# Performance work log

Measured on AMD Instinct MI355X. Metric: run time of the kernel, lower is better.

The kernel has to match this reference:

```python
import jax, jax.numpy as jnp
import numpy as np

B, C, N, D, H, NC = 128, 9, 2048, 192, 384, 18  # batch, in_chans, time, embed, mlp_hidden, classes


def setup_inputs() -> dict:
    key = jax.random.key(0)
    ks = jax.random.split(key, 18)
    rn = lambda k, sh, s=0.02: jax.random.normal(k, sh, dtype=jnp.float32) * s
    return {
        "x": jax.random.normal(ks[0], (B, C, N), dtype=jnp.float32),
        "conv_w": rn(ks[1], (D, C, 3)),
        "conv_b": jnp.zeros((D,), jnp.float32),
        "pos_embed": jnp.zeros((1, N, D), jnp.float32),
        "qkv_w": rn(ks[2], (3 * D, D)),
        "qkv_b": jnp.zeros((3 * D,), jnp.float32),
        "proj_w": rn(ks[3], (D, D)),
        "proj_b": jnp.zeros((D,), jnp.float32),
        "ln1_g": jnp.ones((D,), jnp.float32),
        "ln1_b": jnp.zeros((D,), jnp.float32),
        "mlp_w1": rn(ks[4], (H, D)),
        "mlp_b1": jnp.zeros((H,), jnp.float32),
        "mlp_w2": rn(ks[5], (D, H)),
        "mlp_b2": jnp.zeros((D,), jnp.float32),
        "ln2_g": jnp.ones((D,), jnp.float32),
        "ln2_b": jnp.zeros((D,), jnp.float32),
        "head_w": rn(ks[6], (NC, D)),
        "head_b": jnp.zeros((NC,), jnp.float32),
    }


def _ln(x, g, b, eps=1e-5):
    m = x.mean(-1, keepdims=True)
    v = ((x - m) ** 2).mean(-1, keepdims=True)
    return (x - m) * jax.lax.rsqrt(v + eps) * g + b


def reference(x, conv_w, conv_b, pos_embed, qkv_w, qkv_b, proj_w, proj_b,
              ln1_g, ln1_b, mlp_w1, mlp_b1, mlp_w2, mlp_b2, ln2_g, ln2_b,
              head_w, head_b):
    # patch embed: Conv1d(C->D, k=3, pad=1), then [B, N, D]
    h = jax.lax.conv_general_dilated(
        x, conv_w, window_strides=(1,), padding=[(1, 1)],
        dimension_numbers=("NCH", "OIH", "NCH")) + conv_b[None, :, None]
    h = jnp.transpose(h, (0, 2, 1)) + pos_embed  # [B, N, D]

    # linear (Performer-style) attention with ReLU feature maps
    hn = _ln(h, ln1_g, ln1_b)
    qkv = hn @ qkv_w.T + qkv_b  # [B, N, 3D]
    q, k, v = jnp.split(qkv, 3, axis=-1)
    q = jax.nn.relu(q)
    k = jax.nn.relu(k)
    kv = jnp.einsum("bnd,bne->bde", k, v)       # [B, D, D]
    num = jnp.einsum("bnd,bde->bne", q, kv)      # [B, N, D]
    # NOTE: original sums q over BOTH token and feature dims -> scalar per batch
    denom = q.sum(axis=(1, 2))[:, None, None]
    attn = num / (denom + 1e-6)
    h = h + attn @ proj_w.T + proj_b

    # MLP block (exact GELU, as torch nn.GELU default)
    hn2 = _ln(h, ln2_g, ln2_b)
    m = jax.nn.gelu(hn2 @ mlp_w1.T + mlp_b1, approximate=False)
    h = h + m @ mlp_w2.T + mlp_b2

    # head: AdaptiveAvgPool1d(1) over time, then Linear
    pooled = h.mean(axis=1)  # [B, D]
    return pooled @ head_w.T + head_b  # [B, NC]
```

## Files before the change

### kernel.cpp

```cpp
#include <hip/hip_runtime.h>
#include <cmath>

#define B_   128
#define C_   9
#define N_   2048
#define D_   192
#define H_   384
#define NC_  18

typedef unsigned short ushort_t;
typedef __attribute__((ext_vector_type(8))) __bf16 bf16x8;
typedef __attribute__((ext_vector_type(8))) short short8;
typedef __attribute__((ext_vector_type(16))) float f32x16;

__device__ __forceinline__ ushort_t f2bf(float x) {
    unsigned u = __float_as_uint(x);
    return (ushort_t)((u + 0x7fffu + ((u >> 16) & 1u)) >> 16);
}
__device__ __forceinline__ float bf2f(ushort_t h) {
    return __uint_as_float(((unsigned)h) << 16);
}
__device__ __forceinline__ bf16x8 ldfrag(const ushort_t* p) {
    short8 s = *(const short8*)p;
    return __builtin_bit_cast(bf16x8, s);
}

__global__ __launch_bounds__(192) void conv_k(
    const float* __restrict__ x, const float* __restrict__ w,
    const float* __restrict__ cb, const float* __restrict__ pos,
    float* __restrict__ h)
{
    const int n0 = blockIdx.x * 64;
    const int b  = blockIdx.y;
    const int d  = threadIdx.x;

    __shared__ float xs[C_][66];
    for (int e = threadIdx.x; e < C_ * 66; e += 192) {
        int c = e / 66, i = e % 66;
        int n = n0 - 1 + i;
        xs[c][i] = (n >= 0 && n < N_) ? x[((size_t)b * C_ + c) * N_ + n] : 0.f;
    }
    float wr[C_][3];
#pragma unroll
    for (int c = 0; c < C_; ++c)
#pragma unroll
        for (int t = 0; t < 3; ++t) wr[c][t] = w[(d * C_ + c) * 3 + t];
    const float bias = cb[d];
    __syncthreads();
    for (int i = 0; i < 64; ++i) {
        int n = n0 + i;
        float acc = bias + pos[(size_t)n * D_ + d];
#pragma unroll
        for (int c = 0; c < C_; ++c)
#pragma unroll
            for (int t = 0; t < 3; ++t) acc += xs[c][i + t] * wr[c][t];
        h[((size_t)b * N_ + n) * D_ + d] = acc;
    }
}

__global__ __launch_bounds__(256) void lnsplit_k(
    const float* __restrict__ h, const float* __restrict__ g, const float* __restrict__ b,
    ushort_t* __restrict__ oh, ushort_t* __restrict__ ol)
{
    const int wid = threadIdx.x >> 6, lane = threadIdx.x & 63;
    const size_t row = (size_t)blockIdx.x * 4 + wid;
    const float* hr = h + row * D_;
    float v[3]; float s = 0.f, q = 0.f;
#pragma unroll
    for (int i = 0; i < 3; ++i) { v[i] = hr[lane + i * 64]; s += v[i]; q += v[i] * v[i]; }
#pragma unroll
    for (int o = 32; o > 0; o >>= 1) { s += __shfl_xor(s, o); q += __shfl_xor(q, o); }
    const float m = s * (1.f / D_);
    const float rs = rsqrtf(q * (1.f / D_) - m * m + 1e-5f);
#pragma unroll
    for (int i = 0; i < 3; ++i) {
        int c = lane + i * 64;
        float nv = (v[i] - m) * rs * g[c] + b[c];
        ushort_t hb = f2bf(nv);
        oh[row * D_ + c] = hb;
        ol[row * D_ + c] = f2bf(nv - bf2f(hb));
    }
}

__global__ __launch_bounds__(256) void splitw_k(
    const float* __restrict__ w, ushort_t* __restrict__ hi, ushort_t* __restrict__ lo, int n)
{
    int i = blockIdx.x * 256 + threadIdx.x;
    if (i < n) {
        float v = w[i];
        ushort_t hb = f2bf(v);
        hi[i] = hb;
        lo[i] = f2bf(v - bf2f(hb));
    }
}

template <int EPI, int BM>
__global__ __launch_bounds__(256) void mgemm(
    const ushort_t* __restrict__ Ah, const ushort_t* __restrict__ Al, int K,
    const ushort_t* __restrict__ Wh, const ushort_t* __restrict__ Wl,
    const float* __restrict__ bias, float* __restrict__ dsum,
    ushort_t* __restrict__ oh, ushort_t* __restrict__ ol,
    ushort_t* __restrict__ kTh, ushort_t* __restrict__ kTl,
    ushort_t* __restrict__ vTh, ushort_t* __restrict__ vTl,
    float* __restrict__ facc)
{
    extern __shared__ ushort_t smem[];
    constexpr int MI   = BM / 64;
    constexpr int BUFE = BM * 64 + 12288;
    constexpr int NCH  = 24 + 8 * MI;

    const int tid  = threadIdx.x;
    const int lane = tid & 63;
    const int l5   = lane >> 5;
    const int wid  = tid >> 6;
    const int wr = wid >> 1, wc = wid & 1;
    const int bx = blockIdx.x, by = blockIdx.y;
    const int m0 = bx * BM;

    size_t wbase = 0;
    if (EPI == 0 || EPI == 1) wbase = (size_t)by * 192 * K;
    else if (EPI == 3) wbase = (size_t)(m0 >> 11) * D_ * D_;
    else if (EPI == 4) wbase = (size_t)(bx / 3) * 192 * (size_t)K;
    const ushort_t* Whp = Wh + wbase;
    const ushort_t* Wlp = Wl + wbase;

    int kbeg = 0, kend = K;
    if (EPI == 4) { int seg = K / gridDim.z; kbeg = blockIdx.z * seg; kend = kbeg + seg; }

    auto stage = [&](int buf, int k0) {
        const int base = buf * BUFE;
#pragma unroll
        for (int i = 0; i < NCH / 4; ++i) {
            int c = wid + i * 4;
            const ushort_t* src;
            int dst;
            if (c < 8 * MI) {
                int koct = c & 3, tt = c >> 2;
                int plane = tt & 1, rb = tt >> 1;
                const ushort_t* ap = plane ? Al : Ah;
                src = ap + (size_t)(m0 + rb * 64 + lane) * K + k0 + koct * 8;
                dst = plane * (BM * 32) + koct * (BM * 8) + rb * 512;
            } else {
                int c2 = c - 8 * MI;
                int koct = c2 & 3, tt = c2 >> 2;
                int plane = tt & 1, rb = tt >> 1;
                const ushort_t* wp = plane ? Wlp : Whp;
                src = wp + (size_t)(rb * 64 + lane) * K + k0 + koct * 8;
                dst = BM * 64 + plane * 6144 + koct * 1536 + rb * 512;
            }
            __builtin_amdgcn_global_load_lds(
                (const __attribute__((address_space(1))) void*)src,
                (__attribute__((address_space(3))) void*)(smem + base + dst),
                16, 0, 0);
        }
    };

    f32x16 acc[MI][3] = {};

    const int nt = (kend - kbeg) / 32;
    stage(0, kbeg);
    __syncthreads();
    int cur = 0;
    for (int t = 0; t < nt; ++t) {
        if (t + 1 < nt) stage(cur ^ 1, kbeg + (t + 1) * 32);
        const ushort_t* bb = smem + cur * BUFE;
#pragma unroll
        for (int kh = 0; kh < 2; ++kh) {
            bf16x8 ah[MI], al[MI];
#pragma unroll
            for (int mi = 0; mi < MI; ++mi) {
                int ao = (kh * 2 + l5) * (BM * 8) + (wr * (BM / 2) + mi * 32 + (lane & 31)) * 8;
                ah[mi] = ldfrag(bb + ao);
                al[mi] = ldfrag(bb + BM * 32 + ao);
            }
#pragma unroll
            for (int tn = 0; tn < 3; ++tn) {
                int wo = BM * 64 + (kh * 2 + l5) * 1536 + (wc * 96 + tn * 32 + (lane & 31)) * 8;
                bf16x8 wh = ldfrag(bb + wo);
                bf16x8 wl = ldfrag(bb + wo + 6144);
#pragma unroll
                for (int mi = 0; mi < MI; ++mi) {
                    acc[mi][tn] = __builtin_amdgcn_mfma_f32_32x32x16_bf16(ah[mi], wh, acc[mi][tn], 0, 0, 0);
                    acc[mi][tn] = __builtin_amdgcn_mfma_f32_32x32x16_bf16(ah[mi], wl, acc[mi][tn], 0, 0, 0);
                    acc[mi][tn] = __builtin_amdgcn_mfma_f32_32x32x16_bf16(al[mi], wh, acc[mi][tn], 0, 0, 0);
                }
            }
        }
        __syncthreads();
        cur ^= 1;
    }

    const int cb = wc * 96 + (lane & 31);

    if (EPI == 0) {
        if (by == 0) {
            float qsum = 0.f;
#pragma unroll
            for (int mi = 0; mi < MI; ++mi) {
                const int rb0 = m0 + wr * (BM / 2) + mi * 32 + 4 * l5;
#pragma unroll
                for (int tn = 0; tn < 3; ++tn) {
                    const int col = cb + tn * 32;
                    const float bv = bias[col];
#pragma unroll
                    for (int r = 0; r < 16; ++r) {
                        int row = rb0 + (r & 3) + 8 * (r >> 2);
                        float v = fmaxf(acc[mi][tn][r] + bv, 0.f);
                        qsum += v;
                        ushort_t hb = f2bf(v);
                        oh[(size_t)row * D_ + col] = hb;
                        ol[(size_t)row * D_ + col] = f2bf(v - bf2f(hb));
                    }
                }
            }
            __syncthreads();
            float* red = (float*)smem;
            red[tid] = qsum;
            __syncthreads();
            for (int o = 128; o > 0; o >>= 1) {
                if (tid < o) red[tid] += red[tid + o];
                __syncthreads();
            }
            if (tid == 0) atomicAdd(&dsum[m0 >> 11], red[0]);
        } else {
            ushort_t* dsth = (by == 1) ? kTh : vTh;
            ushort_t* dstl = (by == 1) ? kTl : vTl;
            constexpr int STR = BM + 8;
#pragma unroll
            for (int plane = 0; plane < 2; ++plane) {
                __syncthreads();
#pragma unroll
                for (int mi = 0; mi < MI; ++mi) {
                    const int rl0 = wr * (BM / 2) + mi * 32 + 4 * l5;
#pragma unroll
                    for (int tn = 0; tn < 3; ++tn) {
                        const int col = cb + tn * 32;
                        const float bv = bias[by * 192 + col];
#pragma unroll
                        for (int r = 0; r < 16; ++r) {
                            int rowl = rl0 + (r & 3) + 8 * (r >> 2);
                            float v = acc[mi][tn][r] + bv;
                            if (by == 1) v = fmaxf(v, 0.f);
                            ushort_t hb = f2bf(v);
                            smem[col * STR + rowl] = plane ? f2bf(v - bf2f(hb)) : hb;
                        }
                    }
                }
                __syncthreads();
                if (tid < 192) {
                    ushort_t* dst = plane ? dstl : dsth;
                    size_t gbase = ((size_t)(m0 >> 11) * 192 + tid) * (size_t)N_ + (m0 & 2047);
#pragma unroll
                    for (int i2 = 0; i2 < BM / 8; ++i2)
                        *(uint4*)(dst + gbase + i2 * 8) = *(const uint4*)&smem[tid * STR + i2 * 8];
                }
            }
        }
    } else if (EPI == 1) {
#pragma unroll
        for (int mi = 0; mi < MI; ++mi) {
            const int rb0 = m0 + wr * (BM / 2) + mi * 32 + 4 * l5;
#pragma unroll
            for (int tn = 0; tn < 3; ++tn) {
                const int colg = by * 192 + cb + tn * 32;
                const float bv = bias[colg];
#pragma unroll
                for (int r = 0; r < 16; ++r) {
                    int row = rb0 + (r & 3) + 8 * (r >> 2);
                    float v = acc[mi][tn][r] + bv;
                    float gv = 0.5f * v * (1.f + erff(v * 0.70710678118654752f));
                    ushort_t hb = f2bf(gv);
                    oh[(size_t)row * H_ + colg] = hb;
                    ol[(size_t)row * H_ + colg] = f2bf(gv - bf2f(hb));
                }
            }
        }
    } else if (EPI == 2 || EPI == 3) {
        float s = 1.f;
        if (EPI == 3) s = 1.f / (dsum[m0 >> 11] + 1e-6f);
#pragma unroll
        for (int mi = 0; mi < MI; ++mi) {
            const int rb0 = m0 + wr * (BM / 2) + mi * 32 + 4 * l5;
#pragma unroll
            for (int tn = 0; tn < 3; ++tn) {
                const int col = cb + tn * 32;
                const float bv = bias[col];
#pragma unroll
                for (int r = 0; r < 16; ++r) {
                    int row = rb0 + (r & 3) + 8 * (r >> 2);
                    facc[(size_t)row * D_ + col] += acc[mi][tn][r] * s + bv;
                }
            }
        }
    } else if (EPI == 4) {
#pragma unroll
        for (int mi = 0; mi < MI; ++mi) {
            const int rb0 = m0 + wr * (BM / 2) + mi * 32 + 4 * l5;
#pragma unroll
            for (int tn = 0; tn < 3; ++tn) {
                const int col = cb + tn * 32;
#pragma unroll
                for (int r = 0; r < 16; ++r) {
                    int row = rb0 + (r & 3) + 8 * (r >> 2);
                    atomicAdd(&facc[(size_t)row * D_ + col], acc[mi][tn][r]);
                }
            }
        }
    }
}

__global__ __launch_bounds__(256) void kv2_k(
    const float* __restrict__ pw, const float* __restrict__ kv,
    ushort_t* __restrict__ oh, ushort_t* __restrict__ ol)
{
    __shared__ float As[16][68];
    __shared__ float Ws[16][68];
    const int tid = threadIdx.x;
    const int tx = tid & 15, ty = tid >> 4;
    const int m0 = blockIdx.x * 64;
    const int n0 = blockIdx.y * 64;
    const int b = blockIdx.z;
    const float* kvb = kv + (size_t)b * D_ * D_;
    const int lm = tid >> 2;
    const int lk = (tid & 3) * 4;

    float acc[4][4] = {};
    for (int k0 = 0; k0 < D_; k0 += 16) {
        float4 av = *(const float4*)(pw + (size_t)(m0 + lm) * D_ + k0 + lk);
        As[lk + 0][lm] = av.x; As[lk + 1][lm] = av.y;
        As[lk + 2][lm] = av.z; As[lk + 3][lm] = av.w;
        float4 wv = *(const float4*)(kvb + (size_t)(n0 + lm) * D_ + k0 + lk);
        Ws[lk + 0][lm] = wv.x; Ws[lk + 1][lm] = wv.y;
        Ws[lk + 2][lm] = wv.z; Ws[lk + 3][lm] = wv.w;
        __syncthreads();
#pragma unroll
        for (int kk = 0; kk < 16; ++kk) {
            float4 a4 = *(const float4*)&As[kk][ty * 4];
            float4 w4 = *(const float4*)&Ws[kk][tx * 4];
            float a[4] = {a4.x, a4.y, a4.z, a4.w};
            float w[4] = {w4.x, w4.y, w4.z, w4.w};
#pragma unroll
            for (int i = 0; i < 4; ++i)
#pragma unroll
                for (int j = 0; j < 4; ++j) acc[i][j] += a[i] * w[j];
        }
        __syncthreads();
    }
#pragma unroll
    for (int i = 0; i < 4; ++i) {
        ushort_t hb[4], lb[4];
#pragma unroll
        for (int j = 0; j < 4; ++j) {
            float v = acc[i][j];
            hb[j] = f2bf(v);
            lb[j] = f2bf(v - bf2f(hb[j]));
        }
        size_t base = (size_t)b * D_ * D_ + (size_t)(m0 + ty * 4 + i) * D_ + n0 + tx * 4;
        *(uint2*)&oh[base] = make_uint2((unsigned)hb[0] | ((unsigned)hb[1] << 16),
                                        (unsigned)hb[2] | ((unsigned)hb[3] << 16));
        *(uint2*)&ol[base] = make_uint2((unsigned)lb[0] | ((unsigned)lb[1] << 16),
                                        (unsigned)lb[2] | ((unsigned)lb[3] << 16));
    }
}

__global__ __launch_bounds__(192) void pool_k(
    const float* __restrict__ h, float* __restrict__ pooled)
{
    const int n0 = blockIdx.x * 64;
    const int b  = blockIdx.y;
    const int d  = threadIdx.x;
    const float* hb = h + ((size_t)b * N_ + n0) * D_;
    float s = 0.f;
#pragma unroll 8
    for (int i = 0; i < 64; ++i) s += hb[(size_t)i * D_ + d];
    atomicAdd(pooled + (size_t)b * D_ + d, s);
}

__global__ __launch_bounds__(192) void head_k(
    const float* __restrict__ pooled, const float* __restrict__ hw,
    const float* __restrict__ hb, float* __restrict__ out)
{
    const int b = blockIdx.x, d = threadIdx.x;
    __shared__ float p[D_];
    p[d] = pooled[(size_t)b * D_ + d] * (1.f / N_);
    __syncthreads();
    if (d < NC_) {
        float acc = hb[d];
        for (int e = 0; e < D_; ++e) acc += p[e] * hw[d * D_ + e];
        out[b * NC_ + d] = acc;
    }
}

extern "C" void kernel_launch(void* const* d_in, const int* in_sizes, int n_in,
                              void* d_out, int out_size, void* d_ws, size_t ws_size,
                              hipStream_t stream) {
    (void)in_sizes; (void)n_in; (void)out_size;

    const float* x      = (const float*)d_in[0];
    const float* conv_w = (const float*)d_in[1];
    const float* conv_b = (const float*)d_in[2];
    const float* pos    = (const float*)d_in[3];
    const float* qkv_w  = (const float*)d_in[4];
    const float* qkv_b  = (const float*)d_in[5];
    const float* proj_w = (const float*)d_in[6];
    const float* proj_b = (const float*)d_in[7];
    const float* ln1_g  = (const float*)d_in[8];
    const float* ln1_b  = (const float*)d_in[9];
    const float* mlp_w1 = (const float*)d_in[10];
    const float* mlp_b1 = (const float*)d_in[11];
    const float* mlp_w2 = (const float*)d_in[12];
    const float* mlp_b2 = (const float*)d_in[13];
    const float* ln2_g  = (const float*)d_in[14];
    const float* ln2_b  = (const float*)d_in[15];
    const float* head_w = (const float*)d_in[16];
    const float* head_b = (const float*)d_in[17];
    float* out = (float*)d_out;

    const size_t perB =
        (size_t)N_ * D_ * 4 +
        (size_t)N_ * D_ * 2 * 2 +
        (size_t)N_ * D_ * 2 * 2 +
        (size_t)N_ * D_ * 2 * 4 +
        (size_t)D_ * D_ * 4 +
        (size_t)D_ * D_ * 2 * 2 +
        8192;
    const size_t fixedW = 2ull * (576 * 192 + 384 * 192 + 192 * 384) * 2 + 65536;
    int BC = B_;
    while (BC > 1 && fixedW + (size_t)BC * perB > ws_size) BC >>= 1;
    const int nchunks = B_ / BC;
    const size_t rows = (size_t)BC * N_;

    char* p = (char*)d_ws;
    auto alloc = [&](size_t bytes) -> char* {
        char* r = p;
        p += (bytes + 255) & ~(size_t)255;
        return r;
    };
    ushort_t* qw_hi = (ushort_t*)alloc(576 * 192 * 2);
    ushort_t* qw_lo = (ushort_t*)alloc(576 * 192 * 2);
    ushort_t* w1_hi = (ushort_t*)alloc(384 * 192 * 2);
    ushort_t* w1_lo = (ushort_t*)alloc(384 * 192 * 2);
    ushort_t* w2_hi = (ushort_t*)alloc(192 * 384 * 2);
    ushort_t* w2_lo = (ushort_t*)alloc(192 * 384 * 2);

    const size_t szPl = rows * D_ * 2;
    float*    h      = (float*)alloc(rows * D_ * 4);
    ushort_t* hn_hi  = (ushort_t*)alloc(szPl);
    ushort_t* hn_lo  = (ushort_t*)alloc(szPl);
    ushort_t* q_hi   = (ushort_t*)alloc(szPl);
    ushort_t* q_lo   = (ushort_t*)alloc(szPl);
    ushort_t* kT_hi  = (ushort_t*)alloc(szPl);
    ushort_t* kT_lo  = (ushort_t*)alloc(szPl);
    ushort_t* vT_hi  = (ushort_t*)alloc(szPl);
    ushort_t* vT_lo  = (ushort_t*)alloc(szPl);
    float*    kv     = (float*)alloc((size_t)BC * D_ * D_ * 4);
    ushort_t* kv2t_h = (ushort_t*)alloc((size_t)BC * D_ * D_ * 2);
    ushort_t* kv2t_l = (ushort_t*)alloc((size_t)BC * D_ * D_ * 2);
    float*    dsum   = (float*)alloc((size_t)BC * 4);
    float*    pooled = (float*)alloc((size_t)BC * D_ * 4);
    ushort_t* m_hi   = kT_hi;
    ushort_t* m_lo   = vT_hi;

    splitw_k<<<(576 * 192 + 255) / 256, 256, 0, stream>>>(qkv_w, qw_hi, qw_lo, 576 * 192);
    splitw_k<<<(384 * 192 + 255) / 256, 256, 0, stream>>>(mlp_w1, w1_hi, w1_lo, 384 * 192);
    splitw_k<<<(192 * 384 + 255) / 256, 256, 0, stream>>>(mlp_w2, w2_hi, w2_lo, 192 * 384);

    const int gm = (int)(rows / 128);
    const size_t SH128 = (size_t)(128 * 64 + 12288) * 2 * 2;
    const size_t SH64  = (size_t)(64 * 64 + 12288) * 2 * 2;

    for (int ch = 0; ch < nchunks; ++ch) {
        const int b0 = ch * BC;
        const float* xc = x + (size_t)b0 * C_ * N_;

        hipMemsetAsync(dsum, 0, (size_t)BC * 4, stream);
        hipMemsetAsync(pooled, 0, (size_t)BC * D_ * 4, stream);
        hipMemsetAsync(kv, 0, (size_t)BC * D_ * D_ * 4, stream);

        conv_k<<<dim3(N_ / 64, BC), 192, 0, stream>>>(xc, conv_w, conv_b, pos, h);
        lnsplit_k<<<rows / 4, 256, 0, stream>>>(h, ln1_g, ln1_b, hn_hi, hn_lo);
        mgemm<0, 128><<<dim3(gm, 3), 256, SH128, stream>>>(
            hn_hi, hn_lo, D_, qw_hi, qw_lo, qkv_b, dsum,
            q_hi, q_lo, kT_hi, kT_lo, vT_hi, vT_lo, nullptr);
        mgemm<4, 64><<<dim3(BC * 3, 1, 8), 256, SH64, stream>>>(
            kT_hi, kT_lo, N_, vT_hi, vT_lo, nullptr, nullptr,
            nullptr, nullptr, nullptr, nullptr, nullptr, nullptr, kv);
        kv2_k<<<dim3(3, 3, BC), 256, 0, stream>>>(proj_w, kv, kv2t_h, kv2t_l);
        mgemm<3, 128><<<dim3(gm, 1), 256, SH128, stream>>>(
            q_hi, q_lo, D_, kv2t_h, kv2t_l, proj_b, dsum,
            nullptr, nullptr, nullptr, nullptr, nullptr, nullptr, h);
        lnsplit_k<<<rows / 4, 256, 0, stream>>>(h, ln2_g, ln2_b, hn_hi, hn_lo);
        mgemm<1, 128><<<dim3(gm, 2), 256, SH128, stream>>>(
            hn_hi, hn_lo, D_, w1_hi, w1_lo, mlp_b1, nullptr,
            m_hi, m_lo, nullptr, nullptr, nullptr, nullptr, nullptr);
        mgemm<2, 128><<<dim3(gm, 1), 256, SH128, stream>>>(
            m_hi, m_lo, H_, w2_hi, w2_lo, mlp_b2, nullptr,
            nullptr, nullptr, nullptr, nullptr, nullptr, nullptr, h);
        pool_k<<<dim3(N_ / 64, BC), 192, 0, stream>>>(h, pooled);
        head_k<<<BC, 192, 0, stream>>>(pooled, head_w, head_b, out + (size_t)b0 * NC_);
    }
}
```

Before: 1.695 ms.

## Fuse LayerNorms into conv and proj epilogues, fold pooling into MLP GEMM

Merges LN1 into the conv kernel using a shared-memory tile, and computes LN2 inside the proj GEMM epilogue via cross-lane and LDS reductions. Pooling now accumulates per-column sums in the final MLP GEMM epilogue, which removes the separate lnsplit and pool passes over h. The GEMM K-step shrinks from 32 to 16, cutting LDS per block, and a block-index swizzle changes tile ordering. Costs are smaller K tiles, meaning more barriers per K, plus extra atomics and LDS work in the epilogues.

```diff
diff --git a/kernel.cpp b/kernel.cpp
--- a/kernel.cpp
+++ b/kernel.cpp
@@ -25,16 +25,21 @@
     return __builtin_bit_cast(bf16x8, s);
 }
 
-__global__ __launch_bounds__(192) void conv_k(
+__global__ __launch_bounds__(192) void conv_ln_k(
     const float* __restrict__ x, const float* __restrict__ w,
     const float* __restrict__ cb, const float* __restrict__ pos,
-    float* __restrict__ h)
+    const float* __restrict__ lng, const float* __restrict__ lnb,
+    float* __restrict__ h, ushort_t* __restrict__ oh, ushort_t* __restrict__ ol)
 {
     const int n0 = blockIdx.x * 64;
     const int b  = blockIdx.y;
     const int d  = threadIdx.x;
 
     __shared__ float xs[C_][66];
+    __shared__ float tile[64][193];
+    __shared__ float ps[64][3], pq[64][3];
+    __shared__ float mm[64], rr[64];
+
     for (int e = threadIdx.x; e < C_ * 66; e += 192) {
         int c = e / 66, i = e % 66;
         int n = n0 - 1 + i;
@@ -47,38 +52,46 @@
         for (int t = 0; t < 3; ++t) wr[c][t] = w[(d * C_ + c) * 3 + t];
     const float bias = cb[d];
     __syncthreads();
+
     for (int i = 0; i < 64; ++i) {
-        int n = n0 + i;
-        float acc = bias + pos[(size_t)n * D_ + d];
+        float acc = bias + pos[(size_t)(n0 + i) * D_ + d];
 #pragma unroll
         for (int c = 0; c < C_; ++c)
 #pragma unroll
             for (int t = 0; t < 3; ++t) acc += xs[c][i + t] * wr[c][t];
-        h[((size_t)b * N_ + n) * D_ + d] = acc;
-    }
-}
-
-__global__ __launch_bounds__(256) void lnsplit_k(
-    const float* __restrict__ h, const float* __restrict__ g, const float* __restrict__ b,
-    ushort_t* __restrict__ oh, ushort_t* __restrict__ ol)
-{
-    const int wid = threadIdx.x >> 6, lane = threadIdx.x & 63;
-    const size_t row = (size_t)blockIdx.x * 4 + wid;
-    const float* hr = h + row * D_;
-    float v[3]; float s = 0.f, q = 0.f;
-#pragma unroll
-    for (int i = 0; i < 3; ++i) { v[i] = hr[lane + i * 64]; s += v[i]; q += v[i] * v[i]; }
-#pragma unroll
-    for (int o = 32; o > 0; o >>= 1) { s += __shfl_xor(s, o); q += __shfl_xor(q, o); }
-    const float m = s * (1.f / D_);
-    const float rs = rsqrtf(q * (1.f / D_) - m * m + 1e-5f);
-#pragma unroll
-    for (int i = 0; i < 3; ++i) {
-        int c = lane + i * 64;
-        float nv = (v[i] - m) * rs * g[c] + b[c];
-        ushort_t hb = f2bf(nv);
-        oh[row * D_ + c] = hb;
-        ol[row * D_ + c] = f2bf(nv - bf2f(hb));
+        tile[i][d] = acc;
+    }
+    __syncthreads();
+
+    {
+        int row = threadIdx.x & 63, part = threadIdx.x >> 6;
+        float s = 0.f, q = 0.f;
+        const float* tr = &tile[row][part * 64];
+#pragma unroll 8
+        for (int j = 0; j < 64; ++j) { float v = tr[j]; s += v; q += v * v; }
+        ps[row][part] = s; pq[row][part] = q;
+    }
+    __syncthreads();
+    if (threadIdx.x < 64) {
+        int r = threadIdx.x;
+        float s = ps[r][0] + ps[r][1] + ps[r][2];
+        float q = pq[r][0] + pq[r][1] + pq[r][2];
+        float m = s * (1.f / D_);
+        mm[r] = m;
+        rr[r] = rsqrtf(q * (1.f / D_) - m * m + 1e-5f);
+    }
+    __syncthreads();
+    {
+        const float gd = lng[d], bd = lnb[d];
+        for (int i = 0; i < 64; ++i) {
+            float v = tile[i][d];
+            size_t idx = ((size_t)b * N_ + n0 + i) * D_ + d;
+            h[idx] = v;
+            float nv = (v - mm[i]) * rr[i] * gd + bd;
+            ushort_t hb = f2bf(nv);
+            oh[idx] = hb;
+            ol[idx] = f2bf(nv - bf2f(hb));
+        }
     }
 }
 
@@ -99,22 +112,32 @@
     const ushort_t* __restrict__ Ah, const ushort_t* __restrict__ Al, int K,
     const ushort_t* __restrict__ Wh, const ushort_t* __restrict__ Wl,
     const float* __restrict__ bias, float* __restrict__ dsum,
+    const float* __restrict__ lng, const float* __restrict__ lnb,
     ushort_t* __restrict__ oh, ushort_t* __restrict__ ol,
     ushort_t* __restrict__ kTh, ushort_t* __restrict__ kTl,
     ushort_t* __restrict__ vTh, ushort_t* __restrict__ vTl,
-    float* __restrict__ facc)
+    float* __restrict__ facc, float* __restrict__ pooled)
 {
     extern __shared__ ushort_t smem[];
-    constexpr int MI   = BM / 64;
-    constexpr int BUFE = BM * 64 + 12288;
-    constexpr int NCH  = 24 + 8 * MI;
+    constexpr int MI     = BM / 64;
+    constexpr int APL    = BM * 16;
+    constexpr int AK     = BM * 8;
+    constexpr int AELEMS = BM * 32;
+    constexpr int BUFE   = AELEMS + 6144;
+    constexpr int ACH    = 4 * (BM / 64);
+    constexpr int NCH    = ACH + 12;
 
     const int tid  = threadIdx.x;
     const int lane = tid & 63;
     const int l5   = lane >> 5;
     const int wid  = tid >> 6;
     const int wr = wid >> 1, wc = wid & 1;
-    const int bx = blockIdx.x, by = blockIdx.y;
+    int bx = blockIdx.x;
+    const int by = blockIdx.y;
+    if (EPI != 4) {
+        int nx = gridDim.x;
+        if ((nx & 7) == 0) bx = (bx & 7) * (nx >> 3) + (bx >> 3);
+    }
     const int m0 = bx * BM;
 
     size_t wbase = 0;
@@ -134,19 +157,17 @@
             int c = wid + i * 4;
             const ushort_t* src;
             int dst;
-            if (c < 8 * MI) {
-                int koct = c & 3, tt = c >> 2;
-                int plane = tt & 1, rb = tt >> 1;
+            if (c < ACH) {
+                int koct = c & 1, plane = (c >> 1) & 1, rb = c >> 2;
                 const ushort_t* ap = plane ? Al : Ah;
                 src = ap + (size_t)(m0 + rb * 64 + lane) * K + k0 + koct * 8;
-                dst = plane * (BM * 32) + koct * (BM * 8) + rb * 512;
+                dst = plane * APL + koct * AK + rb * 512;
             } else {
-                int c2 = c - 8 * MI;
-                int koct = c2 & 3, tt = c2 >> 2;
-                int plane = tt & 1, rb = tt >> 1;
+                int c2 = c - ACH;
+                int koct = c2 & 1, plane = (c2 >> 1) & 1, rb = c2 >> 2;
                 const ushort_t* wp = plane ? Wlp : Whp;
                 src = wp + (size_t)(rb * 64 + lane) * K + k0 + koct * 8;
-                dst = BM * 64 + plane * 6144 + koct * 1536 + rb * 512;
+                dst = AELEMS + plane * 3072 + koct * 1536 + rb * 512;
             }
             __builtin_amdgcn_global_load_lds(
                 (const __attribute__((address_space(1))) void*)src,
@@ -157,33 +178,30 @@
 
     f32x16 acc[MI][3] = {};
 
-    const int nt = (kend - kbeg) / 32;
+    const int nt = (kend - kbeg) / 16;
     stage(0, kbeg);
     __syncthreads();
     int cur = 0;
     for (int t = 0; t < nt; ++t) {
-        if (t + 1 < nt) stage(cur ^ 1, kbeg + (t + 1) * 32);
+        if (t + 1 < nt) stage(cur ^ 1, kbeg + (t + 1) * 16);
         const ushort_t* bb = smem + cur * BUFE;
-#pragma unroll
-        for (int kh = 0; kh < 2; ++kh) {
-            bf16x8 ah[MI], al[MI];
+        bf16x8 ah[MI], al[MI];
+#pragma unroll
+        for (int mi = 0; mi < MI; ++mi) {
+            int ao = l5 * AK + (wr * (BM / 2) + mi * 32 + (lane & 31)) * 8;
+            ah[mi] = ldfrag(bb + ao);
+            al[mi] = ldfrag(bb + APL + ao);
+        }
+#pragma unroll
+        for (int tn = 0; tn < 3; ++tn) {
+            int wo = AELEMS + l5 * 1536 + (wc * 96 + tn * 32 + (lane & 31)) * 8;
+            bf16x8 wh = ldfrag(bb + wo);
+            bf16x8 wl = ldfrag(bb + wo + 3072);
 #pragma unroll
             for (int mi = 0; mi < MI; ++mi) {
-                int ao = (kh * 2 + l5) * (BM * 8) + (wr * (BM / 2) + mi * 32 + (lane & 31)) * 8;
-                ah[mi] = ldfrag(bb + ao);
-                al[mi] = ldfrag(bb + BM * 32 + ao);
-            }
-#pragma unroll
-            for (int tn = 0; tn < 3; ++tn) {
-                int wo = BM * 64 + (kh * 2 + l5) * 1536 + (wc * 96 + tn * 32 + (lane & 31)) * 8;
-                bf16x8 wh = ldfrag(bb + wo);
-                bf16x8 wl = ldfrag(bb + wo + 6144);
-#pragma unroll
-                for (int mi = 0; mi < MI; ++mi) {
-                    acc[mi][tn] = __builtin_amdgcn_mfma_f32_32x32x16_bf16(ah[mi], wh, acc[mi][tn], 0, 0, 0);
-                    acc[mi][tn] = __builtin_amdgcn_mfma_f32_32x32x16_bf16(ah[mi], wl, acc[mi][tn], 0, 0, 0);
-                    acc[mi][tn] = __builtin_amdgcn_mfma_f32_32x32x16_bf16(al[mi], wh, acc[mi][tn], 0, 0, 0);
-                }
+                acc[mi][tn] = __builtin_amdgcn_mfma_f32_32x32x16_bf16(ah[mi], wh, acc[mi][tn], 0, 0, 0);
+                acc[mi][tn] = __builtin_amdgcn_mfma_f32_32x32x16_bf16(ah[mi], wl, acc[mi][tn], 0, 0, 0);
+                acc[mi][tn] = __builtin_amdgcn_mfma_f32_32x32x16_bf16(al[mi], wh, acc[mi][tn], 0, 0, 0);
             }
         }
         __syncthreads();
@@ -275,9 +293,8 @@
                 }
             }
         }
-    } else if (EPI == 2 || EPI == 3) {
-        float s = 1.f;
-        if (EPI == 3) s = 1.f / (dsum[m0 >> 11] + 1e-6f);
+    } else if (EPI == 2) {
+        float tsum[3] = {0.f, 0.f, 0.f};
 #pragma unroll
         for (int mi = 0; mi < MI; ++mi) {
             const int rb0 = m0 + wr * (BM / 2) + mi * 32 + 4 * l5;
@@ -288,7 +305,82 @@
 #pragma unroll
                 for (int r = 0; r < 16; ++r) {
                     int row = rb0 + (r & 3) + 8 * (r >> 2);
-                    facc[(size_t)row * D_ + col] += acc[mi][tn][r] * s + bv;
+                    float v = facc[(size_t)row * D_ + col] + acc[mi][tn][r] + bv;
+                    facc[(size_t)row * D_ + col] = v;
+                    tsum[tn] += v;
+                }
+            }
+        }
+#pragma unroll
+        for (int tn = 0; tn < 3; ++tn) {
+            float t = tsum[tn];
+            t += __shfl_xor(t, 32);
+            if (l5 == 0) atomicAdd(&pooled[(size_t)(m0 >> 11) * D_ + cb + tn * 32], t);
+        }
+    } else if (EPI == 3) {
+        const float s = 1.f / (dsum[m0 >> 11] + 1e-6f);
+#pragma unroll
+        for (int mi = 0; mi < MI; ++mi) {
+            const int rb0 = m0 + wr * (BM / 2) + mi * 32 + 4 * l5;
+#pragma unroll
+            for (int tn = 0; tn < 3; ++tn) {
+                const int col = cb + tn * 32;
+                const float bv = bias[col];
+#pragma unroll
+                for (int r = 0; r < 16; ++r) {
+                    int row = rb0 + (r & 3) + 8 * (r >> 2);
+                    float v = facc[(size_t)row * D_ + col] + acc[mi][tn][r] * s + bv;
+                    facc[(size_t)row * D_ + col] = v;
+                    acc[mi][tn][r] = v;
+                }
+            }
+        }
+        float* ls = (float*)smem;
+        float* lq = ls + 256;
+        float* lm = lq + 256;
+        float* lr = lm + 128;
+#pragma unroll
+        for (int mi = 0; mi < MI; ++mi) {
+#pragma unroll
+            for (int r = 0; r < 16; ++r) {
+                float pv = acc[mi][0][r] + acc[mi][1][r] + acc[mi][2][r];
+                float qv = acc[mi][0][r] * acc[mi][0][r] + acc[mi][1][r] * acc[mi][1][r]
+                         + acc[mi][2][r] * acc[mi][2][r];
+#pragma unroll
+                for (int off = 1; off <= 16; off <<= 1) {
+                    pv += __shfl_xor(pv, off);
+                    qv += __shfl_xor(qv, off);
+                }
+                if ((lane & 31) == 0) {
+                    int rl = wr * 64 + mi * 32 + 4 * l5 + (r & 3) + 8 * (r >> 2);
+                    ls[rl * 2 + wc] = pv;
+                    lq[rl * 2 + wc] = qv;
+                }
+            }
+        }
+        __syncthreads();
+        if (tid < 128) {
+            float sv = ls[tid * 2] + ls[tid * 2 + 1];
+            float qv = lq[tid * 2] + lq[tid * 2 + 1];
+            float mv = sv * (1.f / D_);
+            lm[tid] = mv;
+            lr[tid] = rsqrtf(qv * (1.f / D_) - mv * mv + 1e-5f);
+        }
+        __syncthreads();
+#pragma unroll
+        for (int mi = 0; mi < MI; ++mi) {
+#pragma unroll
+            for (int tn = 0; tn < 3; ++tn) {
+                const int col = cb + tn * 32;
+                const float gv = lng[col], bv2 = lnb[col];
+#pragma unroll
+                for (int r = 0; r < 16; ++r) {
+                    int rl = wr * 64 + mi * 32 + 4 * l5 + (r & 3) + 8 * (r >> 2);
+                    float nv = (acc[mi][tn][r] - lm[rl]) * lr[rl] * gv + bv2;
+                    ushort_t hb = f2bf(nv);
+                    size_t idx = (size_t)(m0 + rl) * D_ + col;
+                    oh[idx] = hb;
+                    ol[idx] = f2bf(nv - bf2f(hb));
                 }
             }
         }
@@ -361,19 +453,6 @@
         *(uint2*)&ol[base] = make_uint2((unsigned)lb[0] | ((unsigned)lb[1] << 16),
                                         (unsigned)lb[2] | ((unsigned)lb[3] << 16));
     }
-}
-
-__global__ __launch_bounds__(192) void pool_k(
-    const float* __restrict__ h, float* __restrict__ pooled)
-{
-    const int n0 = blockIdx.x * 64;
-    const int b  = blockIdx.y;
-    const int d  = threadIdx.x;
-    const float* hb = h + ((size_t)b * N_ + n0) * D_;
-    float s = 0.f;
-#pragma unroll 8
-    for (int i = 0; i < 64; ++i) s += hb[(size_t)i * D_ + d];
-    atomicAdd(pooled + (size_t)b * D_ + d, s);
 }
 
 __global__ __launch_bounds__(192) void head_k(
@@ -466,8 +545,9 @@
     splitw_k<<<(192 * 384 + 255) / 256, 256, 0, stream>>>(mlp_w2, w2_hi, w2_lo, 192 * 384);
 
     const int gm = (int)(rows / 128);
-    const size_t SH128 = (size_t)(128 * 64 + 12288) * 2 * 2;
-    const size_t SH64  = (size_t)(64 * 64 + 12288) * 2 * 2;
+    const size_t SH0 = 192 * (128 + 8) * 2;
+    const size_t SHT = (size_t)(128 * 32 + 6144) * 2 * 2;
+    const size_t SH4 = (size_t)(64 * 32 + 6144) * 2 * 2;
 
     for (int ch = 0; ch < nchunks; ++ch) {
         const int b0 = ch * BC;
@@ -477,26 +557,24 @@
         hipMemsetAsync(pooled, 0, (size_t)BC * D_ * 4, stream);
         hipMemsetAsync(kv, 0, (size_t)BC * D_ * D_ * 4, stream);
 
-        conv_k<<<dim3(N_ / 64, BC), 192, 0, stream>>>(xc, conv_w, conv_b, pos, h);
-        lnsplit_k<<<rows / 4, 256, 0, stream>>>(h, ln1_g, ln1_b, hn_hi, hn_lo);
-        mgemm<0, 128><<<dim3(gm, 3), 256, SH128, stream>>>(
-            hn_hi, hn_lo, D_, qw_hi, qw_lo, qkv_b, dsum,
-            q_hi, q_lo, kT_hi, kT_lo, vT_hi, vT_lo, nullptr);
-        mgemm<4, 64><<<dim3(BC * 3, 1, 8), 256, SH64, stream>>>(
-            kT_hi, kT_lo, N_, vT_hi, vT_lo, nullptr, nullptr,
-            nullptr, nullptr, nullptr, nullptr, nullptr, nullptr, kv);
+        conv_ln_k<<<dim3(N_ / 64, BC), 192, 0, stream>>>(
+            xc, conv_w, conv_b, pos, ln1_g, ln1_b, h, hn_hi, hn_lo);
+        mgemm<0, 128><<<dim3(gm, 3), 256, SH0, stream>>>(
+            hn_hi, hn_lo, D_, qw_hi, qw_lo, qkv_b, dsum, nullptr, nullptr,
+            q_hi, q_lo, kT_hi, kT_lo, vT_hi, vT_lo, nullptr, nullptr);
+        mgemm<4, 64><<<dim3(BC * 3, 1, 8), 256, SH4, stream>>>(
+            kT_hi, kT_lo, N_, vT_hi, vT_lo, nullptr, nullptr, nullptr, nullptr,
+            nullptr, nullptr, nullptr, nullptr, nullptr, nullptr, kv, nullptr);
         kv2_k<<<dim3(3, 3, BC), 256, 0, stream>>>(proj_w, kv, kv2t_h, kv2t_l);
-        mgemm<3, 128><<<dim3(gm, 1), 256, SH128, stream>>>(
-            q_hi, q_lo, D_, kv2t_h, kv2t_l, proj_b, dsum,
-            nullptr, nullptr, nullptr, nullptr, nullptr, nullptr, h);
-        lnsplit_k<<<rows / 4, 256, 0, stream>>>(h, ln2_g, ln2_b, hn_hi, hn_lo);
-        mgemm<1, 128><<<dim3(gm, 2), 256, SH128, stream>>>(
-            hn_hi, hn_lo, D_, w1_hi, w1_lo, mlp_b1, nullptr,
-            m_hi, m_lo, nullptr, nullptr, nullptr, nullptr, nullptr);
-        mgemm<2, 128><<<dim3(gm, 1), 256, SH128, stream>>>(
-            m_hi, m_lo, H_, w2_hi, w2_lo, mlp_b2, nullptr,
-            nullptr, nullptr, nullptr, nullptr, nullptr, nullptr, h);
-        pool_k<<<dim3(N_ / 64, BC), 192, 0, stream>>>(h, pooled);
+        mgemm<3, 128><<<dim3(gm, 1), 256, SHT, stream>>>(
+            q_hi, q_lo, D_, kv2t_h, kv2t_l, proj_b, dsum, ln2_g, ln2_b,
+            hn_hi, hn_lo, nullptr, nullptr, nullptr, nullptr, h, nullptr);
+        mgemm<1, 128><<<dim3(gm, 2), 256, SHT, stream>>>(
+            hn_hi, hn_lo, D_, w1_hi, w1_lo, mlp_b1, nullptr, nullptr, nullptr,
+            m_hi, m_lo, nullptr, nullptr, nullptr, nullptr, nullptr, nullptr);
+        mgemm<2, 128><<<dim3(gm, 1), 256, SHT, stream>>>(
+            m_hi, m_lo, H_, w2_hi, w2_lo, mlp_b2, nullptr, nullptr, nullptr,
+            nullptr, nullptr, nullptr, nullptr, nullptr, nullptr, h, pooled);
         head_k<<<BC, 192, 0, stream>>>(pooled, head_w, head_b, out + (size_t)b0 * NC_);
     }
 }
```

New measurement: 2.097 ms. 1.24x slower.
